# Kernel optimization log

Hardware: AMD Instinct MI355X
Metric: run time of the kernel (lower is better)

## Reference

```python
import jax, jax.numpy as jnp
import numpy as np

N_RNA, N_ATAC = 4096, 8192
IN_C, HID, H = 256, 128, 2
DH = HID // H
TOPK, THR = 10, 0.8


def setup_inputs() -> dict:
    key = jax.random.key(0)
    ks = jax.random.split(key, 16)
    s = 0.02
    inp = {
        'x_rna': jax.random.normal(ks[0], (N_RNA, IN_C), jnp.float32),
        'x_atac': jax.random.normal(ks[1], (N_ATAC, IN_C), jnp.float32),
        'chrom_mask': (jax.random.uniform(ks[2], (N_RNA, N_ATAC)) > 0.5).astype(jnp.float32),
        'Wq': jax.random.normal(ks[3], (IN_C, HID)) * s, 'bq': jnp.zeros((HID,)),
        'Wk': jax.random.normal(ks[4], (IN_C, HID)) * s, 'bk': jnp.zeros((HID,)),
        'Wvr': jax.random.normal(ks[5], (IN_C, HID)) * s, 'bvr': jnp.zeros((HID,)),
        'Wva': jax.random.normal(ks[6], (IN_C, HID)) * s, 'bva': jnp.zeros((HID,)),
        'Wor': jax.random.normal(ks[7], (HID, HID)) * s, 'bor': jnp.zeros((HID,)),
        'Woa': jax.random.normal(ks[8], (HID, HID)) * s, 'boa': jnp.zeros((HID,)),
        'Wsr': jax.random.normal(ks[9], (IN_C, HID)) * s, 'bsr': jnp.zeros((HID,)),
        'Wsa': jax.random.normal(ks[10], (IN_C, HID)) * s, 'bsa': jnp.zeros((HID,)),
        'Wdr': jax.random.normal(ks[11], (2 * HID, HID)) * s, 'bdr': jnp.zeros((HID,)),
        'Wda': jax.random.normal(ks[12], (2 * HID, HID)) * s, 'bda': jnp.zeros((HID,)),
    }
    return inp


def reference(x_rna, x_atac, chrom_mask, Wq, bq, Wk, bk, Wvr, bvr, Wva, bva,
              Wor, bor, Woa, boa, Wsr, bsr, Wsa, bsa, Wdr, bdr, Wda, bda):
    # projections -> [N, H, DH]
    q = (x_rna @ Wq + bq).reshape(N_RNA, H, DH)
    k = (x_atac @ Wk + bk).reshape(N_ATAC, H, DH)
    v_a = (x_atac @ Wva + bva).reshape(N_ATAC, H, DH)
    v_r = (x_rna @ Wvr + bvr).reshape(N_RNA, H, DH)

    # raw attention [H, N_rna, N_atac], biological mask, sigmoid
    att = jnp.einsum('rhd,ahd->hra', q, k) * chrom_mask[None]
    att = jax.nn.sigmoid(att)
    thr_mask = (att > THR).astype(att.dtype)

    # top-k sparsify + softmax over selected values, scatter back
    topv, topi = jax.lax.top_k(att, TOPK)          # [H, N_rna, K]
    topv = jax.nn.softmax(topv, axis=-1)
    i_h = jnp.arange(H)[:, None, None]
    i_r = jnp.arange(N_RNA)[None, :, None]
    sparse = jnp.zeros_like(att).at[i_h, i_r, topi].set(topv)
    att = sparse * thr_mask

    # aggregations (second bmm and its transpose)
    rna_agg = jnp.einsum('hra,ahd->rhd', att, v_a).reshape(N_RNA, HID)
    atac_agg = jnp.einsum('hra,rhd->ahd', att, v_r).reshape(N_ATAC, HID)

    # out proj (num_heads > 1), self attention concat, dim reduction
    rna_agg = rna_agg @ Wor + bor
    atac_agg = atac_agg @ Woa + boa
    rna_agg = jnp.concatenate([rna_agg, x_rna @ Wsr + bsr], axis=1)
    atac_agg = jnp.concatenate([atac_agg, x_atac @ Wsa + bsa], axis=1)
    return (rna_agg @ Wdr + bdr, atac_agg @ Wda + bda)
```

## Files before the change

### kernel.cpp

```cpp
#include <hip/hip_runtime.h>
#include <math.h>

#define N_RNA 4096
#define N_ATAC 8192
#define IN_C 256
#define HID 128
#define NH 2
#define TOPK 10
#define CAP 32
#define NCHUNK 8
#define TAU_EPS 0.12f
#define NEG_INF -3.402823466e38f

typedef __attribute__((ext_vector_type(8))) short bf16x8;
typedef __attribute__((ext_vector_type(4))) float f32x4;

static __device__ __forceinline__ f32x4 mfma16(bf16x8 a, bf16x8 b, f32x4 c) {
    return __builtin_amdgcn_mfma_f32_16x16x32_bf16(a, b, c, 0, 0, 0);
}

static __device__ __forceinline__ unsigned short f2bf(float f) {
    unsigned int u = __float_as_uint(f);
    unsigned int r = (u + 0x7fffu + ((u >> 16) & 1u)) >> 16;
    return (unsigned short)r;
}
static __device__ __forceinline__ float bf2f(unsigned short h) {
    return __uint_as_float(((unsigned int)h) << 16);
}

__global__ __launch_bounds__(256) void wprep(
    const float* __restrict__ Wq, const float* __restrict__ Wk,
    const float* __restrict__ Wvr, const float* __restrict__ Wva,
    const float* __restrict__ Wor, const float* __restrict__ bor,
    const float* __restrict__ Woa, const float* __restrict__ boa,
    const float* __restrict__ Wsr, const float* __restrict__ bsr,
    const float* __restrict__ Wsa, const float* __restrict__ bsa,
    const float* __restrict__ Wdr, const float* __restrict__ bdr,
    const float* __restrict__ Wda, const float* __restrict__ bda,
    unsigned short* __restrict__ wt, unsigned short* __restrict__ wrf,
    unsigned short* __restrict__ waf,
    float* __restrict__ brf, float* __restrict__ baf) {
    int bx = blockIdx.x, tid = threadIdx.x;
    if (bx < 32) {
        int cfg = bx >> 3, k0 = (bx & 7) * 32;
        const float* W = (cfg == 0) ? Wq : (cfg == 1) ? Wvr : (cfg == 2) ? Wk : Wva;
        __shared__ float ts[32][132];
#pragma unroll
        for (int rep = 0; rep < 4; ++rep) {
            int id = rep * 256 + tid; int kk = id >> 5, cq = id & 31;
            float4 v = *(const float4*)&W[(size_t)(k0 + kk) * HID + cq * 4];
            ts[kk][cq * 4 + 0] = v.x; ts[kk][cq * 4 + 1] = v.y;
            ts[kk][cq * 4 + 2] = v.z; ts[kk][cq * 4 + 3] = v.w;
        }
        __syncthreads();
        int col = tid >> 1, seg = tid & 1;
        unsigned short hb[16], lb[16];
#pragma unroll
        for (int u = 0; u < 16; ++u) {
            float f = ts[seg * 16 + u][col];
            unsigned short h = f2bf(f);
            hb[u] = h; lb[u] = f2bf(f - bf2f(h));
        }
        unsigned short* hp = wt + cfg * 65536;
        unsigned short* lp = hp + 32768;
        size_t o = (size_t)col * 256 + k0 + seg * 16;
#pragma unroll
        for (int u4 = 0; u4 < 4; ++u4) {
            ushort4 th, tl;
            th.x = hb[u4 * 4]; th.y = hb[u4 * 4 + 1]; th.z = hb[u4 * 4 + 2]; th.w = hb[u4 * 4 + 3];
            tl.x = lb[u4 * 4]; tl.y = lb[u4 * 4 + 1]; tl.z = lb[u4 * 4 + 2]; tl.w = lb[u4 * 4 + 3];
            *(ushort4*)&hp[o + u4 * 4] = th;
            *(ushort4*)&lp[o + u4 * 4] = tl;
        }
        return;
    }
    int f = (bx - 32) * 256 + tid;
    if (f < 16384) {
        int i = f >> 7, j = f & 127; float s = 0.f;
        for (int t = 0; t < 128; ++t) s += Wor[i * 128 + t] * Wdr[t * 128 + j];
        unsigned short h = f2bf(s);
        wrf[(size_t)j * 128 + i] = h;
        wrf[16384 + (size_t)j * 128 + i] = f2bf(s - bf2f(h));
    } else if (f < 49152) {
        int e = f - 16384; int i = e >> 7, j = e & 127; float s = 0.f;
        for (int t = 0; t < 128; ++t) s += Wsr[i * 128 + t] * Wdr[(128 + t) * 128 + j];
        unsigned short h = f2bf(s);
        wrf[32768 + (size_t)j * 256 + i] = h;
        wrf[65536 + (size_t)j * 256 + i] = f2bf(s - bf2f(h));
    } else if (f < 65536) {
        int e = f - 49152; int i = e >> 7, j = e & 127; float s = 0.f;
        for (int t = 0; t < 128; ++t) s += Woa[i * 128 + t] * Wda[t * 128 + j];
        unsigned short h = f2bf(s);
        waf[(size_t)j * 128 + i] = h;
        waf[16384 + (size_t)j * 128 + i] = f2bf(s - bf2f(h));
    } else if (f < 98304) {
        int e = f - 65536; int i = e >> 7, j = e & 127; float s = 0.f;
        for (int t = 0; t < 128; ++t) s += Wsa[i * 128 + t] * Wda[(128 + t) * 128 + j];
        unsigned short h = f2bf(s);
        waf[32768 + (size_t)j * 256 + i] = h;
        waf[65536 + (size_t)j * 256 + i] = f2bf(s - bf2f(h));
    } else if (f < 98432) {
        int j = f - 98304; float s = bdr[j];
        for (int t = 0; t < 128; ++t) s += bor[t] * Wdr[t * 128 + j] + bsr[t] * Wdr[(128 + t) * 128 + j];
        brf[j] = s;
    } else if (f < 98560) {
        int j = f - 98432; float s = bda[j];
        for (int t = 0; t < 128; ++t) s += boa[t] * Wda[t * 128 + j] + bsa[t] * Wda[(128 + t) * 128 + j];
        baf[j] = s;
    }
}

__global__ __launch_bounds__(256) void prep_all(
    const float* __restrict__ mask, unsigned int* __restrict__ bits2,
    float* __restrict__ atac_agg,
    const float* __restrict__ x_rna, const float* __restrict__ x_atac,
    const unsigned short* __restrict__ wt,
    const float* __restrict__ bq, const float* __restrict__ bk,
    const float* __restrict__ bvr, const float* __restrict__ bva,
    unsigned short* __restrict__ qhi, unsigned short* __restrict__ qlo,
    unsigned short* __restrict__ khf_hi, unsigned short* __restrict__ khf_lo,
    float* __restrict__ v_r, float* __restrict__ v_a) {
    __shared__ __align__(16) unsigned short ah_s[32 * 40];
    __shared__ __align__(16) unsigned short al_s[32 * 40];
    int bx = blockIdx.x, tid = threadIdx.x;

    if (bx >= 768 && bx < 1280) {
        int e = bx - 768;
        int rt = e >> 3, ac = e & 7;
        int a0 = ac * 1024 + tid * 4;
        int r0 = rt * 64;
        unsigned int w0[4] = {0, 0, 0, 0}, w1[4] = {0, 0, 0, 0};
#pragma unroll 8
        for (int rr = 0; rr < 32; ++rr) {
            float4 m0 = *(const float4*)&mask[(size_t)(r0 + rr) * N_ATAC + a0];
            float4 m1 = *(const float4*)&mask[(size_t)(r0 + 32 + rr) * N_ATAC + a0];
            w0[0] |= ((m0.x > 0.5f) ? 1u : 0u) << rr;
            w0[1] |= ((m0.y > 0.5f) ? 1u : 0u) << rr;
            w0[2] |= ((m0.z > 0.5f) ? 1u : 0u) << rr;
            w0[3] |= ((m0.w > 0.5f) ? 1u : 0u) << rr;
            w1[0] |= ((m1.x > 0.5f) ? 1u : 0u) << rr;
            w1[1] |= ((m1.y > 0.5f) ? 1u : 0u) << rr;
            w1[2] |= ((m1.z > 0.5f) ? 1u : 0u) << rr;
            w1[3] |= ((m1.w > 0.5f) ? 1u : 0u) << rr;
        }
        uint4 oA = make_uint4(w0[0], w1[0], w0[1], w1[1]);
        uint4 oB = make_uint4(w0[2], w1[2], w0[3], w1[3]);
        *(uint4*)&bits2[((size_t)rt * N_ATAC + a0) * 2] = oA;
        *(uint4*)&bits2[((size_t)rt * N_ATAC + a0) * 2 + 4] = oB;
        return;
    }
    if (bx >= 1280) {
        size_t i = ((size_t)(bx - 1280) * 256 + tid) * 16;
        float4 z = make_float4(0.f, 0.f, 0.f, 0.f);
        *(float4*)&atac_agg[i] = z;
        *(float4*)&atac_agg[i + 4] = z;
        *(float4*)&atac_agg[i + 8] = z;
        *(float4*)&atac_agg[i + 12] = z;
        return;
    }

    int cfg, rblk;
    if (bx < 128)      { cfg = 0; rblk = bx; }
    else if (bx < 256) { cfg = 1; rblk = bx - 128; }
    else if (bx < 512) { cfg = 2; rblk = bx - 256; }
    else               { cfg = 3; rblk = bx - 512; }
    const float* X = (cfg <= 1) ? x_rna : x_atac;
    const float* Bv = (cfg == 0) ? bq : (cfg == 1) ? bvr : (cfg == 2) ? bk : bva;
    const unsigned short* wth = wt + cfg * 65536;
    const unsigned short* wtl = wth + 32768;
    int r0 = rblk * 32;
    int w = tid >> 6, lane = tid & 63, n = lane & 15, quad = lane >> 4;

    const f32x4 zf = {0.f, 0.f, 0.f, 0.f};
    f32x4 acc[2][2];
#pragma unroll
    for (int mt = 0; mt < 2; ++mt)
#pragma unroll
        for (int nt = 0; nt < 2; ++nt) acc[mt][nt] = zf;

    for (int k0 = 0; k0 < IN_C; k0 += 32) {
        __syncthreads();
        {
            int rr = tid >> 3, kq = tid & 7;
            float4 v = *(const float4*)&X[(size_t)(r0 + rr) * IN_C + k0 + kq * 4];
            ushort4 h, l;
            h.x = f2bf(v.x); h.y = f2bf(v.y); h.z = f2bf(v.z); h.w = f2bf(v.w);
            l.x = f2bf(v.x - bf2f(h.x)); l.y = f2bf(v.y - bf2f(h.y));
            l.z = f2bf(v.z - bf2f(h.z)); l.w = f2bf(v.w - bf2f(h.w));
            *(ushort4*)&ah_s[rr * 40 + kq * 4] = h;
            *(ushort4*)&al_s[rr * 40 + kq * 4] = l;
        }
        __syncthreads();
        bf16x8 Afh[2], Afl[2];
#pragma unroll
        for (int mt = 0; mt < 2; ++mt) {
            Afh[mt] = *(const bf16x8*)&ah_s[(mt * 16 + n) * 40 + quad * 8];
            Afl[mt] = *(const bf16x8*)&al_s[(mt * 16 + n) * 40 + quad * 8];
        }
#pragma unroll
        for (int nt = 0; nt < 2; ++nt) {
            int c = w * 32 + nt * 16 + n;
            size_t o = (size_t)c * 256 + k0 + quad * 8;
            bf16x8 Bh = *(const bf16x8*)&wth[o];
            bf16x8 Bl = *(const bf16x8*)&wtl[o];
#pragma unroll
            for (int mt = 0; mt < 2; ++mt) {
                acc[mt][nt] = mfma16(Afh[mt], Bh, acc[mt][nt]);
                acc[mt][nt] = mfma16(Afh[mt], Bl, acc[mt][nt]);
                acc[mt][nt] = mfma16(Afl[mt], Bh, acc[mt][nt]);
            }
        }
    }
    float bvx[2];
    bvx[0] = Bv[w * 32 + n]; bvx[1] = Bv[w * 32 + 16 + n];
    if (cfg == 1 || cfg == 3) {
        float* C = (cfg == 1) ? v_r : v_a;
#pragma unroll
        for (int mt = 0; mt < 2; ++mt)
#pragma unroll
            for (int nt = 0; nt < 2; ++nt)
#pragma unroll
                for (int i = 0; i < 4; ++i) {
                    int r = r0 + mt * 16 + quad * 4 + i;
                    int c = w * 32 + nt * 16 + n;
                    C[(size_t)r * HID + c] = acc[mt][nt][i] + bvx[nt];
                }
    } else if (cfg == 0) {
#pragma unroll
        for (int mt = 0; mt < 2; ++mt)
#pragma unroll
            for (int nt = 0; nt < 2; ++nt)
#pragma unroll
                for (int i = 0; i < 4; ++i) {
                    int r = r0 + mt * 16 + quad * 4 + i;
                    int c = w * 32 + nt * 16 + n;
                    float o = acc[mt][nt][i] + bvx[nt];
                    int head = c >> 6, ch = c & 63;
                    size_t off = ((size_t)head * N_RNA + r) * 64 + ch;
                    unsigned short h = f2bf(o);
                    qhi[off] = h; qlo[off] = f2bf(o - bf2f(h));
                }
    } else {
#pragma unroll
        for (int mt = 0; mt < 2; ++mt)
#pragma unroll
            for (int nt = 0; nt < 2; ++nt)
#pragma unroll
                for (int i = 0; i < 4; ++i) {
                    int r = r0 + mt * 16 + quad * 4 + i;
                    int c = w * 32 + nt * 16 + n;
                    float o = acc[mt][nt][i] + bvx[nt];
                    int head = c >> 6, ch = c & 63;
                    size_t off = ((size_t)(head * 512 + (r >> 4)) * 8 + (ch >> 3)) * 128
                               + (size_t)(r & 15) * 8 + (ch & 7);
                    unsigned short h = f2bf(o);
                    khf_hi[off] = h; khf_lo[off] = f2bf(o - bf2f(h));
                }
    }
}

__global__ __launch_bounds__(256, 4) void attn2(
    const unsigned short* __restrict__ qhi, const unsigned short* __restrict__ qlo,
    const unsigned short* __restrict__ khf_hi, const unsigned short* __restrict__ khf_lo,
    const unsigned int* __restrict__ bits2,
    int* __restrict__ scnt, float* __restrict__ sval, int* __restrict__ sidx) {
    int hq = blockIdx.x; int h = hq >> 3, chunk = hq & 7;
    int rt = blockIdx.y; int r0 = rt * 32;
    int tid = threadIdx.x;
    int w = tid >> 6, lane = tid & 63;
    int n = lane & 15, quad = lane >> 4;
    int q4 = quad * 4;
    int at0 = chunk * 64 + w * 16;
    int hbase = h * 512;
    int rt64 = rt >> 1, word = rt & 1;

    __shared__ __align__(16) float smem[32 * 65];
    __shared__ float taus[32];
    __shared__ int   lcnt[32];

    const bf16x8* kh8 = (const bf16x8*)khf_hi;
    const bf16x8* kl8 = (const bf16x8*)khf_lo;

    bf16x8 Ah[2][2], Al[2][2];
#pragma unroll
    for (int mt = 0; mt < 2; ++mt)
#pragma unroll
        for (int c = 0; c < 2; ++c) {
            size_t off = ((size_t)h * N_RNA + r0 + mt * 16 + n) * 64 + c * 32 + quad * 8;
            Ah[mt][c] = *(const bf16x8*)(qhi + off);
            Al[mt][c] = *(const bf16x8*)(qlo + off);
        }

    float mx[2][4];
#pragma unroll
    for (int mt = 0; mt < 2; ++mt)
#pragma unroll
        for (int i = 0; i < 4; ++i) mx[mt][i] = 0.f;

#pragma unroll 2
    for (int t = 0; t < 16; ++t) {
        int at = at0 + t;
        size_t bidx = ((size_t)hbase + at) * 128 + lane;
        bf16x8 Bh0 = kh8[bidx];
        bf16x8 Bh1 = kh8[bidx + 64];
        unsigned int bw = bits2[((size_t)rt64 * N_ATAC + at * 16 + n) * 2 + word];

        f32x4 S[2];
#pragma unroll
        for (int mt = 0; mt < 2; ++mt) {
            f32x4 s = {0.f, 0.f, 0.f, 0.f};
            s = mfma16(Ah[mt][0], Bh0, s);
            s = mfma16(Ah[mt][1], Bh1, s);
            S[mt] = s;
        }
#pragma unroll
        for (int mt = 0; mt < 2; ++mt) {
            unsigned int sh = bw >> ((mt << 4) + q4);
#pragma unroll
            for (int i = 0; i < 4; ++i) {
                float v = ((sh >> i) & 1) ? S[mt][i] : 0.f;
                mx[mt][i] = fmaxf(mx[mt][i], v);
            }
        }
    }

    {
        int b = w * 16 + n;
#pragma unroll
        for (int mt = 0; mt < 2; ++mt)
#pragma unroll
            for (int i = 0; i < 4; ++i) smem[(mt * 16 + q4 + i) * 65 + b] = mx[mt][i];
    }
    __syncthreads();
    {
        int row = tid >> 3, sub = tid & 7;
        float v[8];
#pragma unroll
        for (int j = 0; j < 8; ++j) v[j] = smem[row * 65 + sub * 8 + j];
        float t10 = 0.f;
#pragma unroll
        for (int s = 0; s < 10; ++s) {
            float bv = v[0]; int bj = 0;
#pragma unroll
            for (int j = 1; j < 8; ++j) if (v[j] > bv) { bv = v[j]; bj = j; }
            int meta = (sub << 3) | bj;
#pragma unroll
            for (int off = 1; off < 8; off <<= 1) {
                float ov = __shfl_xor(bv, off);
                int om = __shfl_xor(meta, off);
                if (ov > bv || (ov == bv && om < meta)) { bv = ov; meta = om; }
            }
            if ((meta >> 3) == sub) v[meta & 7] = -1.f;
            t10 = bv;
        }
        if (sub == 0) taus[row] = t10 - TAU_EPS;
        if (tid < 32) lcnt[tid] = 0;
    }
    __syncthreads();

    float tau[2][4];
#pragma unroll
    for (int mt = 0; mt < 2; ++mt)
#pragma unroll
        for (int i = 0; i < 4; ++i) tau[mt][i] = taus[mt * 16 + q4 + i];

    float* lval = smem;
    int*   lidx = (int*)(smem + 1024);

#pragma unroll 2
    for (int t = 0; t < 16; ++t) {
        int at = at0 + t;
        size_t bidx = ((size_t)hbase + at) * 128 + lane;
        bf16x8 Bh0 = kh8[bidx];
        bf16x8 Bh1 = kh8[bidx + 64];
        bf16x8 Bl0 = kl8[bidx];
        bf16x8 Bl1 = kl8[bidx + 64];
        unsigned int bw = bits2[((size_t)rt64 * N_ATAC + at * 16 + n) * 2 + word];

        f32x4 S[2];
#pragma unroll
        for (int mt = 0; mt < 2; ++mt) {
            f32x4 s = {0.f, 0.f, 0.f, 0.f};
            s = mfma16(Ah[mt][0], Bh0, s);
            s = mfma16(Ah[mt][1], Bh1, s);
            s = mfma16(Ah[mt][0], Bl0, s);
            s = mfma16(Ah[mt][1], Bl1, s);
            s = mfma16(Al[mt][0], Bh0, s);
            s = mfma16(Al[mt][1], Bh1, s);
            S[mt] = s;
        }
        int a16 = at * 16 + n;
#pragma unroll
        for (int mt = 0; mt < 2; ++mt) {
            unsigned int sh = bw >> ((mt << 4) + q4);
#pragma unroll
            for (int i = 0; i < 4; ++i) {
                if (((sh >> i) & 1) && S[mt][i] >= tau[mt][i]) {
                    int row = mt * 16 + q4 + i;
                    int pos = atomicAdd(&lcnt[row], 1);
                    if (pos < CAP) { lval[row * CAP + pos] = S[mt][i]; lidx[row * CAP + pos] = a16; }
                }
            }
        }
    }
    __syncthreads();

    if (tid < 32) {
        int c = lcnt[tid]; if (c > CAP) c = CAP;
        scnt[((size_t)h * N_RNA + r0 + tid) * NCHUNK + chunk] = c;
    }
    {
        int row = tid >> 3, j0 = tid & 7;
        int c = lcnt[row]; if (c > CAP) c = CAP;
        size_t slot = ((size_t)h * N_RNA + r0 + row) * NCHUNK + chunk;
        for (int j = j0; j < c; j += 8) {
            sval[slot * CAP + j] = lval[row * CAP + j];
            sidx[slot * CAP + j] = lidx[row * CAP + j];
        }
    }
}

__global__ __launch_bounds__(256) void fin_agg(
    const int* __restrict__ scnt, const float* __restrict__ sval, const int* __restrict__ sidx,
    const float* __restrict__ v_a, const float* __restrict__ v_r,
    float* __restrict__ rna_agg, float* __restrict__ atac_agg) {
    int wid = threadIdx.x >> 6, lane = threadIdx.x & 63;
    int p = blockIdx.x * 4 + wid;
    int h = p >> 12, r = p & 4095;
    size_t sbase = (size_t)p * NCHUNK;

    float val[4]; int aidx[4];
#pragma unroll
    for (int j = 0; j < 4; ++j) {
        int e = j * 64 + lane;
        int chunk = e >> 5, pos = e & 31;
        int c = scnt[sbase + chunk];
        size_t sl = (sbase + chunk) * CAP + pos;
        bool ok = pos < c;
        val[j] = ok ? sval[sl] : NEG_INF;
        aidx[j] = ok ? sidx[sl] : 0;
    }

    float sv[10]; int si[10];
#pragma unroll
    for (int s = 0; s < 10; ++s) {
        float bv = val[0]; int bj = 0;
#pragma unroll
        for (int j = 1; j < 4; ++j) if (val[j] > bv) { bv = val[j]; bj = j; }
        int bmeta = (bj << 6) | lane;
#pragma unroll
        for (int off = 32; off >= 1; off >>= 1) {
            float ov = __shfl_xor(bv, off);
            int om = __shfl_xor(bmeta, off);
            if (ov > bv || (ov == bv && om < bmeta)) { bv = ov; bmeta = om; }
        }
        int wj = bmeta >> 6, wl = bmeta & 63;
        if (lane == wl) {
#pragma unroll
            for (int j = 0; j < 4; ++j) if (j == wj) val[j] = NEG_INF;
        }
        int av = aidx[0];
#pragma unroll
        for (int j = 1; j < 4; ++j) if (wj == j) av = aidx[j];
        sv[s] = bv;
        si[s] = __shfl(av, wl);
    }

    float wgt[10]; float sum = 0.f; float sg[10];
#pragma unroll
    for (int s = 0; s < 10; ++s) {
        sg[s] = 1.0f / (1.0f + expf(-sv[s]));
        float es = expf(sg[s]);
        wgt[s] = es;
        sum += es;
    }
    float inv = 1.0f / sum;
#pragma unroll
    for (int s = 0; s < 10; ++s) {
        wgt[s] *= inv;
        if (!(sg[s] > 0.8f)) wgt[s] = 0.f;
    }

    float acc = 0.f;
#pragma unroll
    for (int s = 0; s < 10; ++s) {
        float vv = v_a[(size_t)si[s] * HID + h * 64 + lane];
        acc += wgt[s] * vv;
    }
    rna_agg[(size_t)r * HID + h * 64 + lane] = acc;

    float vr = v_r[(size_t)r * HID + h * 64 + lane];
#pragma unroll
    for (int s = 0; s < 10; ++s) {
        if (wgt[s] != 0.f) {
            atomicAdd(&atac_agg[(size_t)si[s] * HID + h * 64 + lane], wgt[s] * vr);
        }
    }
}

__global__ __launch_bounds__(256) void out_gemm(
    const float* __restrict__ rna_agg, const float* __restrict__ x_rna,
    const unsigned short* __restrict__ wrt, const float* __restrict__ brf,
    const float* __restrict__ atac_agg, const float* __restrict__ x_atac,
    const unsigned short* __restrict__ wat, const float* __restrict__ baf,
    float* __restrict__ out_r, float* __restrict__ out_a) {
    __shared__ __align__(16) unsigned short ah_s[32 * 40];
    __shared__ __align__(16) unsigned short al_s[32 * 40];
    int bx = blockIdx.x, tid = threadIdx.x;
    const float *A, *X, *bias; const unsigned short* wb; float* C; int r0;
    if (bx < 128) { A = rna_agg; X = x_rna; wb = wrt; bias = brf; C = out_r; r0 = bx * 32; }
    else { A = atac_agg; X = x_atac; wb = wat; bias = baf; C = out_a; r0 = (bx - 128) * 32; }
    int w = tid >> 6, lane = tid & 63, n = lane & 15, quad = lane >> 4;

    const f32x4 zf = {0.f, 0.f, 0.f, 0.f};
    f32x4 acc[2][2];
#pragma unroll
    for (int mt = 0; mt < 2; ++mt)
#pragma unroll
        for (int nt = 0; nt < 2; ++nt) acc[mt][nt] = zf;

    for (int k0 = 0; k0 < 384; k0 += 32) {
        __syncthreads();
        {
            int rr = tid >> 3, kq = tid & 7;
            float4 v;
            if (k0 < 128) v = *(const float4*)&A[(size_t)(r0 + rr) * HID + k0 + kq * 4];
            else          v = *(const float4*)&X[(size_t)(r0 + rr) * IN_C + (k0 - 128) + kq * 4];
            ushort4 h, l;
            h.x = f2bf(v.x); h.y = f2bf(v.y); h.z = f2bf(v.z); h.w = f2bf(v.w);
            l.x = f2bf(v.x - bf2f(h.x)); l.y = f2bf(v.y - bf2f(h.y));
            l.z = f2bf(v.z - bf2f(h.z)); l.w = f2bf(v.w - bf2f(h.w));
            *(ushort4*)&ah_s[rr * 40 + kq * 4] = h;
            *(ushort4*)&al_s[rr * 40 + kq * 4] = l;
        }
        __syncthreads();
        bf16x8 Afh[2], Afl[2];
#pragma unroll
        for (int mt = 0; mt < 2; ++mt) {
            Afh[mt] = *(const bf16x8*)&ah_s[(mt * 16 + n) * 40 + quad * 8];
            Afl[mt] = *(const bf16x8*)&al_s[(mt * 16 + n) * 40 + quad * 8];
        }
#pragma unroll
        for (int nt = 0; nt < 2; ++nt) {
            int c = w * 32 + nt * 16 + n;
            size_t o;
            const unsigned short *ph, *pl;
            if (k0 < 128) { o = (size_t)c * 128 + k0 + quad * 8;         ph = wb;         pl = wb + 16384; }
            else          { o = (size_t)c * 256 + (k0 - 128) + quad * 8; ph = wb + 32768; pl = wb + 65536; }
            bf16x8 Bh = *(const bf16x8*)&ph[o];
            bf16x8 Bl = *(const bf16x8*)&pl[o];
#pragma unroll
            for (int mt = 0; mt < 2; ++mt) {
                acc[mt][nt] = mfma16(Afh[mt], Bh, acc[mt][nt]);
                acc[mt][nt] = mfma16(Afh[mt], Bl, acc[mt][nt]);
                acc[mt][nt] = mfma16(Afl[mt], Bh, acc[mt][nt]);
            }
        }
    }
    float bvx[2];
    bvx[0] = bias[w * 32 + n]; bvx[1] = bias[w * 32 + 16 + n];
#pragma unroll
    for (int mt = 0; mt < 2; ++mt)
#pragma unroll
        for (int nt = 0; nt < 2; ++nt)
#pragma unroll
            for (int i = 0; i < 4; ++i) {
                int r = r0 + mt * 16 + quad * 4 + i;
                int c = w * 32 + nt * 16 + n;
                C[(size_t)r * HID + c] = acc[mt][nt][i] + bvx[nt];
            }
}

extern "C" void kernel_launch(void* const* d_in, const int* in_sizes, int n_in,
                              void* d_out, int out_size, void* d_ws, size_t ws_size,
                              hipStream_t stream) {
    const float* x_rna = (const float*)d_in[0];
    const float* x_atac = (const float*)d_in[1];
    const float* mask = (const float*)d_in[2];
    const float* Wq = (const float*)d_in[3];  const float* bq = (const float*)d_in[4];
    const float* Wk = (const float*)d_in[5];  const float* bk = (const float*)d_in[6];
    const float* Wvr = (const float*)d_in[7]; const float* bvr = (const float*)d_in[8];
    const float* Wva = (const float*)d_in[9]; const float* bva = (const float*)d_in[10];
    const float* Wor = (const float*)d_in[11]; const float* bor = (const float*)d_in[12];
    const float* Woa = (const float*)d_in[13]; const float* boa = (const float*)d_in[14];
    const float* Wsr = (const float*)d_in[15]; const float* bsr = (const float*)d_in[16];
    const float* Wsa = (const float*)d_in[17]; const float* bsa = (const float*)d_in[18];
    const float* Wdr = (const float*)d_in[19]; const float* bdr = (const float*)d_in[20];
    const float* Wda = (const float*)d_in[21]; const float* bda = (const float*)d_in[22];

    float* out_r = (float*)d_out;
    float* out_a = out_r + N_RNA * HID;

    float* ws = (float*)d_ws;
    unsigned short* qhi = (unsigned short*)ws;
    unsigned short* qlo = qhi + 524288;
    unsigned short* khf_hi = qlo + 524288;
    unsigned short* khf_lo = khf_hi + 1048576;
    unsigned int* bits2 = (unsigned int*)(ws + 1572864);
    float* v_r = ws + 1572864 + 1048576;
    float* v_a = v_r + 524288;
    float* Wr1 = v_a + 1048576;
    float* Wr2 = Wr1 + 16384;
    float* brf = Wr2 + 32768;
    float* Wa1 = brf + 128;
    float* Wa2 = Wa1 + 16384;
    float* baf = Wa2 + 32768;
    int* scnt = (int*)(baf + 128);
    float* sval = (float*)scnt + 65536;
    int* sidx = (int*)(sval + 2097152);
    float* rna_agg = (float*)sidx + 2097152;
    float* atac_agg = rna_agg + 524288;
    unsigned short* wt = (unsigned short*)(atac_agg + 1048576);

    unsigned short* wrf = (unsigned short*)Wr1;
    unsigned short* waf = (unsigned short*)Wa1;

    hipLaunchKernelGGL(wprep, dim3(417), dim3(256), 0, stream,
                       Wq, Wk, Wvr, Wva,
                       Wor, bor, Woa, boa, Wsr, bsr, Wsa, bsa, Wdr, bdr, Wda, bda,
                       wt, wrf, waf, brf, baf);
    hipLaunchKernelGGL(prep_all, dim3(1536), dim3(256), 0, stream,
                       mask, bits2, atac_agg, x_rna, x_atac, wt,
                       bq, bk, bvr, bva,
                       qhi, qlo, khf_hi, khf_lo, v_r, v_a);
    hipLaunchKernelGGL(attn2, dim3(16, 128), dim3(256), 0, stream,
                       qhi, qlo, khf_hi, khf_lo, bits2, scnt, sval, sidx);
    hipLaunchKernelGGL(fin_agg, dim3(2048), dim3(256), 0, stream,
                       scnt, sval, sidx, v_a, v_r, rna_agg, atac_agg);
    hipLaunchKernelGGL(out_gemm, dim3(384), dim3(256), 0, stream,
                       rna_agg, x_rna, wrf, brf,
                       atac_agg, x_atac, waf, baf, out_r, out_a);
}
```

Before: 380.8 us.

## Screen candidates with single bf16 MFMA and rescore exactly in fp32

The attention screening pass now uses only the high bf16 halves of q and k, one MFMA pair per tile instead of the three-product hi/lo split. It records only candidate indices. The finalize kernel then recomputes each candidate's score in fp32 from new fp32 copies of q and k, using a wave-wide dot product and shuffle reduction. This removes two thirds of the screening MFMAs, the lo-part loads, and the score-value buffer. The costs are serial per-candidate rescoring with 6-step shuffle reductions in fin_agg, plus relying on the threshold margin to absorb the larger bf16 screening error.

```diff
diff --git a/kernel.cpp b/kernel.cpp
--- a/kernel.cpp
+++ b/kernel.cpp
@@ -117,8 +117,8 @@
     const unsigned short* __restrict__ wt,
     const float* __restrict__ bq, const float* __restrict__ bk,
     const float* __restrict__ bvr, const float* __restrict__ bva,
-    unsigned short* __restrict__ qhi, unsigned short* __restrict__ qlo,
-    unsigned short* __restrict__ khf_hi, unsigned short* __restrict__ khf_lo,
+    unsigned short* __restrict__ qhi, unsigned short* __restrict__ khf_hi,
+    float* __restrict__ q_f32, float* __restrict__ k_f32,
     float* __restrict__ v_r, float* __restrict__ v_a) {
     __shared__ __align__(16) unsigned short ah_s[32 * 40];
     __shared__ __align__(16) unsigned short al_s[32 * 40];
@@ -237,8 +237,8 @@
                     float o = acc[mt][nt][i] + bvx[nt];
                     int head = c >> 6, ch = c & 63;
                     size_t off = ((size_t)head * N_RNA + r) * 64 + ch;
-                    unsigned short h = f2bf(o);
-                    qhi[off] = h; qlo[off] = f2bf(o - bf2f(h));
+                    qhi[off] = f2bf(o);
+                    q_f32[(size_t)r * HID + c] = o;
                 }
     } else {
 #pragma unroll
@@ -253,17 +253,16 @@
                     int head = c >> 6, ch = c & 63;
                     size_t off = ((size_t)(head * 512 + (r >> 4)) * 8 + (ch >> 3)) * 128
                                + (size_t)(r & 15) * 8 + (ch & 7);
-                    unsigned short h = f2bf(o);
-                    khf_hi[off] = h; khf_lo[off] = f2bf(o - bf2f(h));
+                    khf_hi[off] = f2bf(o);
+                    k_f32[(size_t)r * HID + c] = o;
                 }
     }
 }
 
 __global__ __launch_bounds__(256, 4) void attn2(
-    const unsigned short* __restrict__ qhi, const unsigned short* __restrict__ qlo,
-    const unsigned short* __restrict__ khf_hi, const unsigned short* __restrict__ khf_lo,
+    const unsigned short* __restrict__ qhi, const unsigned short* __restrict__ khf_hi,
     const unsigned int* __restrict__ bits2,
-    int* __restrict__ scnt, float* __restrict__ sval, int* __restrict__ sidx) {
+    int* __restrict__ scnt, int* __restrict__ sidx) {
     int hq = blockIdx.x; int h = hq >> 3, chunk = hq & 7;
     int rt = blockIdx.y; int r0 = rt * 32;
     int tid = threadIdx.x;
@@ -279,16 +278,14 @@
     __shared__ int   lcnt[32];
 
     const bf16x8* kh8 = (const bf16x8*)khf_hi;
-    const bf16x8* kl8 = (const bf16x8*)khf_lo;
-
-    bf16x8 Ah[2][2], Al[2][2];
+
+    bf16x8 Ah[2][2];
 #pragma unroll
     for (int mt = 0; mt < 2; ++mt)
 #pragma unroll
         for (int c = 0; c < 2; ++c) {
             size_t off = ((size_t)h * N_RNA + r0 + mt * 16 + n) * 64 + c * 32 + quad * 8;
             Ah[mt][c] = *(const bf16x8*)(qhi + off);
-            Al[mt][c] = *(const bf16x8*)(qlo + off);
         }
 
     float mx[2][4];
@@ -364,8 +361,7 @@
 #pragma unroll
         for (int i = 0; i < 4; ++i) tau[mt][i] = taus[mt * 16 + q4 + i];
 
-    float* lval = smem;
-    int*   lidx = (int*)(smem + 1024);
+    int* lidx = (int*)smem;
 
 #pragma unroll 2
     for (int t = 0; t < 16; ++t) {
@@ -373,8 +369,6 @@
         size_t bidx = ((size_t)hbase + at) * 128 + lane;
         bf16x8 Bh0 = kh8[bidx];
         bf16x8 Bh1 = kh8[bidx + 64];
-        bf16x8 Bl0 = kl8[bidx];
-        bf16x8 Bl1 = kl8[bidx + 64];
         unsigned int bw = bits2[((size_t)rt64 * N_ATAC + at * 16 + n) * 2 + word];
 
         f32x4 S[2];
@@ -383,10 +377,6 @@
             f32x4 s = {0.f, 0.f, 0.f, 0.f};
             s = mfma16(Ah[mt][0], Bh0, s);
             s = mfma16(Ah[mt][1], Bh1, s);
-            s = mfma16(Ah[mt][0], Bl0, s);
-            s = mfma16(Ah[mt][1], Bl1, s);
-            s = mfma16(Al[mt][0], Bh0, s);
-            s = mfma16(Al[mt][1], Bh1, s);
             S[mt] = s;
         }
         int a16 = at * 16 + n;
@@ -398,7 +388,7 @@
                 if (((sh >> i) & 1) && S[mt][i] >= tau[mt][i]) {
                     int row = mt * 16 + q4 + i;
                     int pos = atomicAdd(&lcnt[row], 1);
-                    if (pos < CAP) { lval[row * CAP + pos] = S[mt][i]; lidx[row * CAP + pos] = a16; }
+                    if (pos < CAP) lidx[row * CAP + pos] = a16;
                 }
             }
         }
@@ -414,14 +404,14 @@
         int c = lcnt[row]; if (c > CAP) c = CAP;
         size_t slot = ((size_t)h * N_RNA + r0 + row) * NCHUNK + chunk;
         for (int j = j0; j < c; j += 8) {
-            sval[slot * CAP + j] = lval[row * CAP + j];
             sidx[slot * CAP + j] = lidx[row * CAP + j];
         }
     }
 }
 
 __global__ __launch_bounds__(256) void fin_agg(
-    const int* __restrict__ scnt, const float* __restrict__ sval, const int* __restrict__ sidx,
+    const int* __restrict__ scnt, const int* __restrict__ sidx,
+    const float* __restrict__ q_f32, const float* __restrict__ k_f32,
     const float* __restrict__ v_a, const float* __restrict__ v_r,
     float* __restrict__ rna_agg, float* __restrict__ atac_agg) {
     int wid = threadIdx.x >> 6, lane = threadIdx.x & 63;
@@ -429,16 +419,25 @@
     int h = p >> 12, r = p & 4095;
     size_t sbase = (size_t)p * NCHUNK;
 
+    int cnt[8];
+#pragma unroll
+    for (int ch = 0; ch < 8; ++ch) cnt[ch] = scnt[sbase + ch];
+    float qv = q_f32[(size_t)r * HID + h * 64 + lane];
+
     float val[4]; int aidx[4];
 #pragma unroll
-    for (int j = 0; j < 4; ++j) {
-        int e = j * 64 + lane;
-        int chunk = e >> 5, pos = e & 31;
-        int c = scnt[sbase + chunk];
-        size_t sl = (sbase + chunk) * CAP + pos;
-        bool ok = pos < c;
-        val[j] = ok ? sval[sl] : NEG_INF;
-        aidx[j] = ok ? sidx[sl] : 0;
+    for (int j = 0; j < 4; ++j) { val[j] = NEG_INF; aidx[j] = 0; }
+
+#pragma unroll
+    for (int ch = 0; ch < 8; ++ch) {
+        int c = cnt[ch];
+        for (int pos = 0; pos < c; ++pos) {
+            int a = sidx[(sbase + ch) * CAP + pos];
+            float s = qv * k_f32[(size_t)a * HID + h * 64 + lane];
+#pragma unroll
+            for (int off = 1; off < 64; off <<= 1) s += __shfl_xor(s, off);
+            if (lane == ((ch & 1) * 32 + pos)) { val[ch >> 1] = s; aidx[ch >> 1] = a; }
+        }
     }
 
     float sv[10]; int si[10];
@@ -593,27 +592,21 @@
 
     float* ws = (float*)d_ws;
     unsigned short* qhi = (unsigned short*)ws;
-    unsigned short* qlo = qhi + 524288;
-    unsigned short* khf_hi = qlo + 524288;
-    unsigned short* khf_lo = khf_hi + 1048576;
-    unsigned int* bits2 = (unsigned int*)(ws + 1572864);
-    float* v_r = ws + 1572864 + 1048576;
+    unsigned short* khf_hi = qhi + 524288;
+    float* q_f32 = ws + 786432;
+    float* k_f32 = q_f32 + 524288;
+    unsigned int* bits2 = (unsigned int*)(k_f32 + 1048576);
+    float* v_r = (float*)bits2 + 1048576;
     float* v_a = v_r + 524288;
-    float* Wr1 = v_a + 1048576;
-    float* Wr2 = Wr1 + 16384;
-    float* brf = Wr2 + 32768;
-    float* Wa1 = brf + 128;
-    float* Wa2 = Wa1 + 16384;
-    float* baf = Wa2 + 32768;
+    unsigned short* wrf = (unsigned short*)(v_a + 1048576);
+    float* brf = v_a + 1048576 + 49152;
+    unsigned short* waf = (unsigned short*)(brf + 128);
+    float* baf = brf + 128 + 49152;
     int* scnt = (int*)(baf + 128);
-    float* sval = (float*)scnt + 65536;
-    int* sidx = (int*)(sval + 2097152);
-    float* rna_agg = (float*)sidx + 2097152;
+    int* sidx = scnt + 65536;
+    float* rna_agg = (float*)(sidx + 2097152);
     float* atac_agg = rna_agg + 524288;
     unsigned short* wt = (unsigned short*)(atac_agg + 1048576);
-
-    unsigned short* wrf = (unsigned short*)Wr1;
-    unsigned short* waf = (unsigned short*)Wa1;
 
     hipLaunchKernelGGL(wprep, dim3(417), dim3(256), 0, stream,
                        Wq, Wk, Wvr, Wva,
@@ -622,11 +615,11 @@
     hipLaunchKernelGGL(prep_all, dim3(1536), dim3(256), 0, stream,
                        mask, bits2, atac_agg, x_rna, x_atac, wt,
                        bq, bk, bvr, bva,
-                       qhi, qlo, khf_hi, khf_lo, v_r, v_a);
+                       qhi, khf_hi, q_f32, k_f32, v_r, v_a);
     hipLaunchKernelGGL(attn2, dim3(16, 128), dim3(256), 0, stream,
-                       qhi, qlo, khf_hi, khf_lo, bits2, scnt, sval, sidx);
+                       qhi, khf_hi, bits2, scnt, sidx);
     hipLaunchKernelGGL(fin_agg, dim3(2048), dim3(256), 0, stream,
-                       scnt, sval, sidx, v_a, v_r, rna_agg, atac_agg);
+                       scnt, sidx, q_f32, k_f32, v_a, v_r, rna_agg, atac_agg);
     hipLaunchKernelGGL(out_gemm, dim3(384), dim3(256), 0, stream,
                        rna_agg, x_rna, wrf, brf,
                        atac_agg, x_atac, waf, baf, out_r, out_a);
```

Measured after the change: 499.2 us. 31.1% more time.
